# Performance work log

Measured on AMD Instinct MI355X. Metric: run time of the kernel, lower is better.

The kernel has to match this reference:

```python
import jax, jax.numpy as jnp
import numpy as np

N_NODES = 4096
N_EDGES = 32768
PE_DIM = 16
HIDDEN = 128


def setup_inputs() -> dict:
    key = jax.random.key(0)
    k_nodes, k_send, k_recv, k_w = jax.random.split(key, 4)
    nodes = jax.random.normal(k_nodes, (N_NODES, 8), dtype=jnp.float32)
    senders = jax.random.randint(k_send, (N_EDGES,), 0, N_NODES)
    receivers = jax.random.randint(k_recv, (N_EDGES,), 0, N_NODES)
    W = jax.random.normal(k_w, (PE_DIM, HIDDEN), dtype=jnp.float32) / np.sqrt(PE_DIM).astype(np.float32)
    b = jnp.zeros((HIDDEN,), dtype=jnp.float32)
    return {"nodes": nodes, "senders": senders, "receivers": receivers, "W": W, "b": b}


def reference(nodes, senders, receivers, W, b):
    n = nodes.shape[0]
    pe_dim = W.shape[0]
    # out-degree per node (clamped at 1, as in the original)
    ones = jnp.ones(senders.shape[0], dtype=jnp.float32)
    degree = jnp.maximum(jax.ops.segment_sum(ones, senders, num_segments=n), 1.0)
    inv_deg_e = (1.0 / degree)[senders]  # [E], per-edge 1/deg(sender)

    prob = jnp.eye(n, dtype=jnp.float32)  # [n, n] landing probabilities
    diags = []
    for _ in range(pe_dim):
        # gather sender rows, normalize, scatter-add into receiver rows
        msg = prob[senders] * inv_deg_e[:, None]           # [E, n]
        prob = jax.ops.segment_sum(msg, receivers, num_segments=n)  # [n, n]
        diags.append(jnp.diagonal(prob))                    # return probability A^k_ii
    pe = jnp.stack(diags, axis=-1)  # [n, pe_dim]
    return pe @ W + b               # [n, hidden]
```

## Files before the change

kernel.cpp:

```cpp
#include <hip/hip_runtime.h>

#define NN 4096
#define NE 32768
#define PED 16
#define HID 128
#define CW 16
#define NCHUNK 64
#define THREADS 1024
#define PASSES 4

typedef _Float16 h_t;
typedef _Float16 h8 __attribute__((ext_vector_type(8)));

__device__ __forceinline__ int xbyte(int s) {
  int g = ((s & 3) << 1) | ((s >> 2) & 1);
  return ((s >> 2) << 7) + (g << 4);
}


__global__ void count_kernel(const int* __restrict__ senders,
                             const int* __restrict__ receivers,
                             int* __restrict__ outdeg, int* __restrict__ indeg) {
  int e = blockIdx.x * blockDim.x + threadIdx.x;
  if (e < NE) {
    atomicAdd(&outdeg[senders[e]], 1);
    atomicAdd(&indeg[receivers[e]], 1);
  }
}

__global__ void deg_inv_kernel(const int* __restrict__ outdeg, float* __restrict__ dinv) {
  int i = blockIdx.x * blockDim.x + threadIdx.x;
  if (i < NN) {
    int d = outdeg[i];
    if (d < 1) d = 1;
    dinv[i] = 1.0f / (float)d;
  }
}

__global__ void sort_kernel(const int* __restrict__ indeg,
                            int* __restrict__ rowperm, int* __restrict__ sortpos,
                            int* __restrict__ chunk_off, int* __restrict__ chunk_max) {
  __shared__ int hist[64];
  __shared__ int base[64];
  int t = threadIdx.x;
  if (t < 64) hist[t] = 0;
  __syncthreads();
  for (int r = t; r < NN; r += 256) {
    int d = indeg[r]; if (d > 63) d = 63;
    atomicAdd(&hist[d], 1);
  }
  __syncthreads();
  if (t == 0) {
    int acc = 0;
    for (int i = 0; i < 64; ++i) { base[i] = acc; acc += hist[i]; }
  }
  __syncthreads();
  for (int r = t; r < NN; r += 256) {
    int d = indeg[r]; if (d > 63) d = 63;
    int pos = atomicAdd(&base[d], 1);
    rowperm[pos] = r;
    sortpos[r] = pos;
  }
  __syncthreads();
  if (t < NCHUNK) {
    int m = 0;
    for (int i = 0; i < 64; ++i) {
      int d = indeg[rowperm[(t << 6) + i]];
      if (d > m) m = d;
    }
    chunk_max[t] = m;
  }
  __syncthreads();
  if (t == 0) {
    int acc = 0;
    for (int c = 0; c < NCHUNK; ++c) { chunk_off[c] = acc; acc += chunk_max[c] << 6; }
    chunk_off[NCHUNK] = acc;
  }
}

__global__ void zero_ell(const int* __restrict__ chunk_off,
                         int2* __restrict__ e1, int2* __restrict__ e2) {
  int total = chunk_off[NCHUNK] + 256;
  int stride = gridDim.x * blockDim.x;
  for (int i = blockIdx.x * blockDim.x + threadIdx.x; i < total; i += stride) {
    e1[i] = make_int2(0, 0);
    e2[i] = make_int2(0, 0);
  }
}

__global__ void fill_ell(const int* __restrict__ senders, const int* __restrict__ receivers,
                         const int* __restrict__ sortpos, const int* __restrict__ chunk_off,
                         const float* __restrict__ dinv, int* __restrict__ fillc,
                         int2* __restrict__ ell) {
  int e = blockIdx.x * blockDim.x + threadIdx.x;
  if (e < NE) {
    int r = receivers[e], s = senders[e];
    int p = sortpos[r];
    int tslot = atomicAdd(&fillc[r], 1);
    int slot = chunk_off[p >> 6] + (tslot << 6) + (p & 63);
    ell[slot] = make_int2(xbyte(s), __float_as_int(dinv[s]));
  }
}

__global__ void sort_ell(const int* __restrict__ chunk_off,
                         const int* __restrict__ chunk_max,
                         const int2* __restrict__ src, int2* __restrict__ dst) {
  int p = blockIdx.x * blockDim.x + threadIdx.x;
  int c = p >> 6, l = p & 63;
  int base = chunk_off[c], maxd = chunk_max[c];
  if (maxd > 200) {
    for (int t = 0; t < maxd; ++t) dst[base + (t << 6) + l] = src[base + (t << 6) + l];
    return;
  }
  unsigned long long cnt = 0;
  for (int t = 0; t < maxd; ++t) {
    int2 e = src[base + (t << 6) + l];
    int cl = (((e.x >> 4) & 7) - l) & 7;
    cnt += 1ull << (cl << 3);
  }
  unsigned long long pre = 0;
  for (int k = 1; k < 8; ++k) pre += cnt << (k << 3);
  unsigned long long used = 0;
  for (int t = 0; t < maxd; ++t) {
    int2 e = src[base + (t << 6) + l];
    int cl = (((e.x >> 4) & 7) - l) & 7;
    int pos = (int)(((pre + used) >> (cl << 3)) & 255);
    used += 1ull << (cl << 3);
    dst[base + (pos << 6) + l] = e;
  }
}


__global__ __launch_bounds__(THREADS, 4)
void fused_kernel(const int2* __restrict__ ell,
                  const int* __restrict__ chunk_off,
                  const int* __restrict__ chunk_max,
                  const int* __restrict__ rowperm,
                  float* __restrict__ pe) {
  __shared__ __align__(16) h_t X[NN * CW];
  char* Xb = (char*)X;
  int c0 = blockIdx.x * CW;
  int tid = threadIdx.x;
  int wave = tid >> 6, lane = tid & 63;

  for (int s = tid; s < NN; s += THREADS) {
    int d = s - c0;
    h8 lo, hi;
#pragma unroll
    for (int j = 0; j < 8; ++j) {
      lo[j] = (h_t)((d == j) ? 1.0f : 0.0f);
      hi[j] = (h_t)((d == 8 + j) ? 1.0f : 0.0f);
    }
    int xb = xbyte(s);
    *reinterpret_cast<h8*>(Xb + xb) = lo;
    *reinterpret_cast<h8*>(Xb + (xb ^ 16)) = hi;
  }
  __syncthreads();

  for (int k = 0; k < PED; ++k) {
    h8 rlo[PASSES], rhi[PASSES];
    int rxb[PASSES];
#pragma unroll
    for (int pass = 0; pass < PASSES; ++pass) {
      int chunk = (pass << 4) + ((pass & 1) ? (15 - wave) : wave);
      int base = chunk_off[chunk];
      int maxd = chunk_max[chunk];
      int r = rowperm[(chunk << 6) + lane];
      rxb[pass] = xbyte(r);
      float a[16];
#pragma unroll
      for (int j = 0; j < 16; ++j) a[j] = 0.f;
      const int2* ep = ell + base + lane;
      int2 cw = ep[0];
      int2 n1 = ep[64];
      h8 lo = *reinterpret_cast<const h8*>(Xb + cw.x);
      h8 hi = *reinterpret_cast<const h8*>(Xb + (cw.x ^ 16));
      for (int t = 0; t < maxd; ++t) {
        int2 n2 = ep[128];
        ep += 64;
        h8 nlo = *reinterpret_cast<const h8*>(Xb + n1.x);
        h8 nhi = *reinterpret_cast<const h8*>(Xb + (n1.x ^ 16));
        float w = __int_as_float(cw.y);
#pragma unroll
        for (int j = 0; j < 8; ++j) {
          a[j]     = fmaf((float)lo[j], w, a[j]);
          a[8 + j] = fmaf((float)hi[j], w, a[8 + j]);
        }
        cw = n1; n1 = n2; lo = nlo; hi = nhi;
      }
      h8 plo, phi;
#pragma unroll
      for (int j = 0; j < 8; ++j) { plo[j] = (h_t)a[j]; phi[j] = (h_t)a[8 + j]; }
      rlo[pass] = plo; rhi[pass] = phi;
      int dj = r - c0;
      if (dj >= 0 && dj < CW) {
        float dv = a[0];
#pragma unroll
        for (int j = 1; j < 16; ++j) dv = (dj == j) ? a[j] : dv;
        pe[r * PED + k] = dv;
      }
    }
    __syncthreads();
#pragma unroll
    for (int pass = 0; pass < PASSES; ++pass) {
      int xb = rxb[pass];
      *reinterpret_cast<h8*>(Xb + xb) = rlo[pass];
      *reinterpret_cast<h8*>(Xb + (xb ^ 16)) = rhi[pass];
    }
    __syncthreads();
  }
}

__global__ void out_kernel(const float* __restrict__ pe, const float* __restrict__ W,
                           const float* __restrict__ bvec, float* __restrict__ out) {
  __shared__ float sW[PED * HID];
  int r = blockIdx.x;
  int h = threadIdx.x;
  for (int i = h; i < PED * HID; i += HID) sW[i] = W[i];
  __syncthreads();
  float acc = bvec[h];
  float p[PED];
#pragma unroll
  for (int kk = 0; kk < PED; ++kk) p[kk] = pe[r * PED + kk];
#pragma unroll
  for (int kk = 0; kk < PED; ++kk) acc = fmaf(p[kk], sW[kk * HID + h], acc);
  out[r * HID + h] = acc;
}

extern "C" void kernel_launch(void* const* d_in, const int* in_sizes, int n_in,
                              void* d_out, int out_size, void* d_ws, size_t ws_size,
                              hipStream_t stream) {
  const int* senders = (const int*)d_in[1];
  const int* receivers = (const int*)d_in[2];
  const float* W = (const float*)d_in[3];
  const float* bvec = (const float*)d_in[4];
  float* out = (float*)d_out;

  char* p = (char*)d_ws;
  int* outdeg = (int*)p;    p += (size_t)NN * 4;
  int* indeg = (int*)p;     p += (size_t)NN * 4;
  int* fillc = (int*)p;     p += (size_t)NN * 4;
  float* dinv = (float*)p;  p += (size_t)NN * 4;
  int* rowperm = (int*)p;   p += (size_t)NN * 4;
  int* sortpos = (int*)p;   p += (size_t)NN * 4;
  int* chunk_off = (int*)p; p += 128 * 4;
  int* chunk_max = (int*)p; p += 128 * 4;
  float* pe = (float*)p;    p += (size_t)NN * PED * 4;
  size_t ell_slots = (size_t)64 * NE + 256;
  int2* ell = (int2*)p;     p += ell_slots * sizeof(int2);
  int2* ell2 = (int2*)p;

  hipMemsetAsync(d_ws, 0, (size_t)NN * 4 * 3, stream);
  count_kernel<<<NE / 256, 256, 0, stream>>>(senders, receivers, outdeg, indeg);
  deg_inv_kernel<<<NN / 256, 256, 0, stream>>>(outdeg, dinv);
  sort_kernel<<<1, 256, 0, stream>>>(indeg, rowperm, sortpos, chunk_off, chunk_max);
  zero_ell<<<256, 256, 0, stream>>>(chunk_off, ell, ell2);
  fill_ell<<<NE / 256, 256, 0, stream>>>(senders, receivers, sortpos, chunk_off, dinv, fillc, ell);
  sort_ell<<<NN / 256, 256, 0, stream>>>(chunk_off, chunk_max, ell, ell2);

  fused_kernel<<<NN / CW, THREADS, 0, stream>>>(ell2, chunk_off, chunk_max, rowperm, pe);

  out_kernel<<<NN, HID, 0, stream>>>(pe, W, bvec, out);
}
```

Before: 214.6 us.

## Merge setup kernels, schedule ELL slots for LDS banks, use fma_mix in SpMM loop

Folds the inverse-degree computation into the sort kernel and replaces the full ELL zeroing with a small tail zero. Padding slots are now written explicitly with bank-staggered dummy entries. Edges are rescheduled so each slot index lines up with a target LDS bank group, aiming to reduce bank conflicts in the fused kernel. The inner SpMM loop now uses v_fma_mix_f32 inline asm, which reads fp16 halves directly without separate conversions, and prefetches one more edge ahead. The cost is a more complex scheduling kernel and reliance on hand-written ISA.

Result: faster. 206.2 us (-3.9%).

```diff
diff --git a/kernel.cpp b/kernel.cpp
--- a/kernel.cpp
+++ b/kernel.cpp
@@ -28,16 +28,8 @@
   }
 }
 
-__global__ void deg_inv_kernel(const int* __restrict__ outdeg, float* __restrict__ dinv) {
-  int i = blockIdx.x * blockDim.x + threadIdx.x;
-  if (i < NN) {
-    int d = outdeg[i];
-    if (d < 1) d = 1;
-    dinv[i] = 1.0f / (float)d;
-  }
-}
-
-__global__ void sort_kernel(const int* __restrict__ indeg,
+__global__ void sort_kernel(const int* __restrict__ indeg, const int* __restrict__ outdeg,
+                            float* __restrict__ dinv,
                             int* __restrict__ rowperm, int* __restrict__ sortpos,
                             int* __restrict__ chunk_off, int* __restrict__ chunk_max) {
   __shared__ int hist[64];
@@ -48,6 +40,8 @@
   for (int r = t; r < NN; r += 256) {
     int d = indeg[r]; if (d > 63) d = 63;
     atomicAdd(&hist[d], 1);
+    int od = outdeg[r]; if (od < 1) od = 1;
+    dinv[r] = 1.0f / (float)od;
   }
   __syncthreads();
   if (t == 0) {
@@ -78,14 +72,9 @@
   }
 }
 
-__global__ void zero_ell(const int* __restrict__ chunk_off,
-                         int2* __restrict__ e1, int2* __restrict__ e2) {
-  int total = chunk_off[NCHUNK] + 256;
-  int stride = gridDim.x * blockDim.x;
-  for (int i = blockIdx.x * blockDim.x + threadIdx.x; i < total; i += stride) {
-    e1[i] = make_int2(0, 0);
-    e2[i] = make_int2(0, 0);
-  }
+__global__ void zero_tail(const int* __restrict__ chunk_off, int2* __restrict__ e2) {
+  int total = chunk_off[NCHUNK];
+  e2[total + threadIdx.x] = make_int2(0, 0);
 }
 
 __global__ void fill_ell(const int* __restrict__ senders, const int* __restrict__ receivers,
@@ -102,34 +91,53 @@
   }
 }
 
-__global__ void sort_ell(const int* __restrict__ chunk_off,
-                         const int* __restrict__ chunk_max,
-                         const int2* __restrict__ src, int2* __restrict__ dst) {
+__global__ void sched_ell(const int* __restrict__ chunk_off,
+                          const int* __restrict__ chunk_max,
+                          const int* __restrict__ rowperm,
+                          const int* __restrict__ indeg,
+                          const int2* __restrict__ src, int2* __restrict__ dst) {
   int p = blockIdx.x * blockDim.x + threadIdx.x;
   int c = p >> 6, l = p & 63;
   int base = chunk_off[c], maxd = chunk_max[c];
-  if (maxd > 200) {
-    for (int t = 0; t < maxd; ++t) dst[base + (t << 6) + l] = src[base + (t << 6) + l];
+  int d = indeg[rowperm[p]];
+  if (maxd > 63) {
+    for (int t = 0; t < d; ++t) dst[base + (t << 6) + l] = src[base + (t << 6) + l];
+    for (int t = d; t < maxd; ++t)
+      dst[base + (t << 6) + l] = make_int2(((t + l) & 7) << 4, 0);
     return;
   }
-  unsigned long long cnt = 0;
-  for (int t = 0; t < maxd; ++t) {
+  unsigned long long occ = 0;
+  int placed[8] = {0, 0, 0, 0, 0, 0, 0, 0};
+  for (int t = 0; t < d; ++t) {
     int2 e = src[base + (t << 6) + l];
     int cl = (((e.x >> 4) & 7) - l) & 7;
-    cnt += 1ull << (cl << 3);
-  }
-  unsigned long long pre = 0;
-  for (int k = 1; k < 8; ++k) pre += cnt << (k << 3);
-  unsigned long long used = 0;
-  for (int t = 0; t < maxd; ++t) {
+    int slot = cl + (placed[cl]++ << 3);
+    if (slot < maxd) { dst[base + (slot << 6) + l] = e; occ |= 1ull << slot; }
+  }
+  int placed2[8] = {0, 0, 0, 0, 0, 0, 0, 0};
+  for (int t = 0; t < d; ++t) {
     int2 e = src[base + (t << 6) + l];
     int cl = (((e.x >> 4) & 7) - l) & 7;
-    int pos = (int)(((pre + used) >> (cl << 3)) & 255);
-    used += 1ull << (cl << 3);
-    dst[base + (pos << 6) + l] = e;
-  }
-}
-
+    int slot = cl + (placed2[cl]++ << 3);
+    if (slot >= maxd) {
+      int f = __builtin_ctzll(~occ & ((1ull << maxd) - 1));
+      dst[base + (f << 6) + l] = e;
+      occ |= 1ull << f;
+    }
+  }
+  unsigned long long rem = ~occ & ((1ull << maxd) - 1);
+  while (rem) {
+    int slot = __builtin_ctzll(rem);
+    rem &= rem - 1;
+    dst[base + (slot << 6) + l] = make_int2(((slot + l) & 7) << 4, 0);
+  }
+}
+
+
+#define MIXL(acc, srcv) \
+  asm("v_fma_mix_f32 %0, %1, %2, %0 op_sel_hi:[1,0,0]" : "+v"(acc) : "v"(srcv), "v"(w))
+#define MIXH(acc, srcv) \
+  asm("v_fma_mix_f32 %0, %1, %2, %0 op_sel:[1,0,0] op_sel_hi:[1,0,0]" : "+v"(acc) : "v"(srcv), "v"(w))
 
 __global__ __launch_bounds__(THREADS, 4)
 void fused_kernel(const int2* __restrict__ ell,
@@ -144,16 +152,16 @@
   int wave = tid >> 6, lane = tid & 63;
 
   for (int s = tid; s < NN; s += THREADS) {
-    int d = s - c0;
-    h8 lo, hi;
+    int dd = s - c0;
+    h8 lo8, hi8;
 #pragma unroll
     for (int j = 0; j < 8; ++j) {
-      lo[j] = (h_t)((d == j) ? 1.0f : 0.0f);
-      hi[j] = (h_t)((d == 8 + j) ? 1.0f : 0.0f);
+      lo8[j] = (h_t)((dd == j) ? 1.0f : 0.0f);
+      hi8[j] = (h_t)((dd == 8 + j) ? 1.0f : 0.0f);
     }
     int xb = xbyte(s);
-    *reinterpret_cast<h8*>(Xb + xb) = lo;
-    *reinterpret_cast<h8*>(Xb + (xb ^ 16)) = hi;
+    *reinterpret_cast<h8*>(Xb + xb) = lo8;
+    *reinterpret_cast<h8*>(Xb + (xb ^ 16)) = hi8;
   }
   __syncthreads();
 
@@ -171,22 +179,26 @@
 #pragma unroll
       for (int j = 0; j < 16; ++j) a[j] = 0.f;
       const int2* ep = ell + base + lane;
-      int2 cw = ep[0];
-      int2 n1 = ep[64];
-      h8 lo = *reinterpret_cast<const h8*>(Xb + cw.x);
-      h8 hi = *reinterpret_cast<const h8*>(Xb + (cw.x ^ 16));
+      int2 e0 = ep[0];
+      int2 e1 = ep[64];
+      int2 e2 = ep[128];
+      int4 lo = *reinterpret_cast<const int4*>(Xb + e0.x);
+      int4 hi = *reinterpret_cast<const int4*>(Xb + (e0.x ^ 16));
       for (int t = 0; t < maxd; ++t) {
-        int2 n2 = ep[128];
+        int2 e3 = ep[192];
         ep += 64;
-        h8 nlo = *reinterpret_cast<const h8*>(Xb + n1.x);
-        h8 nhi = *reinterpret_cast<const h8*>(Xb + (n1.x ^ 16));
-        float w = __int_as_float(cw.y);
-#pragma unroll
-        for (int j = 0; j < 8; ++j) {
-          a[j]     = fmaf((float)lo[j], w, a[j]);
-          a[8 + j] = fmaf((float)hi[j], w, a[8 + j]);
-        }
-        cw = n1; n1 = n2; lo = nlo; hi = nhi;
+        int4 nlo = *reinterpret_cast<const int4*>(Xb + e1.x);
+        int4 nhi = *reinterpret_cast<const int4*>(Xb + (e1.x ^ 16));
+        float w = __int_as_float(e0.y);
+        MIXL(a[0], lo.x);  MIXH(a[1], lo.x);
+        MIXL(a[2], lo.y);  MIXH(a[3], lo.y);
+        MIXL(a[4], lo.z);  MIXH(a[5], lo.z);
+        MIXL(a[6], lo.w);  MIXH(a[7], lo.w);
+        MIXL(a[8], hi.x);  MIXH(a[9], hi.x);
+        MIXL(a[10], hi.y); MIXH(a[11], hi.y);
+        MIXL(a[12], hi.z); MIXH(a[13], hi.z);
+        MIXL(a[14], hi.w); MIXH(a[15], hi.w);
+        e0 = e1; e1 = e2; e2 = e3; lo = nlo; hi = nhi;
       }
       h8 plo, phi;
 #pragma unroll
@@ -252,11 +264,10 @@
 
   hipMemsetAsync(d_ws, 0, (size_t)NN * 4 * 3, stream);
   count_kernel<<<NE / 256, 256, 0, stream>>>(senders, receivers, outdeg, indeg);
-  deg_inv_kernel<<<NN / 256, 256, 0, stream>>>(outdeg, dinv);
-  sort_kernel<<<1, 256, 0, stream>>>(indeg, rowperm, sortpos, chunk_off, chunk_max);
-  zero_ell<<<256, 256, 0, stream>>>(chunk_off, ell, ell2);
+  sort_kernel<<<1, 256, 0, stream>>>(indeg, outdeg, dinv, rowperm, sortpos, chunk_off, chunk_max);
+  zero_tail<<<1, 256, 0, stream>>>(chunk_off, ell2);
   fill_ell<<<NE / 256, 256, 0, stream>>>(senders, receivers, sortpos, chunk_off, dinv, fillc, ell);
-  sort_ell<<<NN / 256, 256, 0, stream>>>(chunk_off, chunk_max, ell, ell2);
+  sched_ell<<<NN / 256, 256, 0, stream>>>(chunk_off, chunk_max, rowperm, indeg, ell, ell2);
 
   fused_kernel<<<NN / CW, THREADS, 0, stream>>>(ell2, chunk_off, chunk_max, rowperm, pe);
 
```
